# Performance work log

Hardware: AMD Instinct MI355X
Metric: run time of the kernel (lower is better)

The kernel has to match this reference:

```python
import jax, jax.numpy as jnp
import numpy as np

N_NODES = 100000
N_EDGES = 1_600_000
IN_DIM, HID, OUT_DIM, N_BLOCKS = 963, 192, 3, 6


def spmm(src, dst, w, x):
    # sparse adj @ x, adj[dst, src] = w  (COO edge list)
    msgs = x[src] * w[:, None]                      # [E, F]
    return jax.ops.segment_sum(msgs, dst, num_segments=N_NODES)


def gconv(x, src, dst, ew, w, lw, b):
    # Pixel2Mesh GConv: adj @ (x @ W) + x @ W_loop + b
    return spmm(src, dst, ew, x @ w) + x @ lw + b


def setup_inputs() -> dict:
    key = jax.random.key(0)
    ks = jax.random.split(key, 13)
    s = 0.02  # small init scale to keep deep stack numerically tame
    return {
        "inputs": jax.random.normal(ks[0], (N_NODES, IN_DIM), jnp.float32),
        "edge_src": jax.random.randint(ks[1], (N_EDGES,), 0, N_NODES),
        "edge_dst": jax.random.randint(ks[2], (N_EDGES,), 0, N_NODES),
        "edge_weight": jax.random.uniform(ks[3], (N_EDGES,), jnp.float32) / 16.0,
        "w_in": jax.random.normal(ks[4], (IN_DIM, HID), jnp.float32) * s,
        "loop_in": jax.random.normal(ks[5], (IN_DIM, HID), jnp.float32) * s,
        "b_in": jnp.zeros((HID,), jnp.float32),
        "blocks_w": jax.random.normal(ks[6], (N_BLOCKS, 2, HID, HID), jnp.float32) * s,
        "blocks_loop": jax.random.normal(ks[7], (N_BLOCKS, 2, HID, HID), jnp.float32) * s,
        "blocks_b": jnp.zeros((N_BLOCKS, 2, HID), jnp.float32),
        "w_out": jax.random.normal(ks[8], (HID, OUT_DIM), jnp.float32) * s,
        "loop_out": jax.random.normal(ks[9], (HID, OUT_DIM), jnp.float32) * s,
        "b_out": jnp.zeros((OUT_DIM,), jnp.float32),
    }


def reference(inputs, edge_src, edge_dst, edge_weight, w_in, loop_in, b_in,
              blocks_w, blocks_loop, blocks_b, w_out, loop_out, b_out):
    x = gconv(inputs, edge_src, edge_dst, edge_weight, w_in, loop_in, b_in)

    def block(x, params):
        bw, bl, bb = params
        h = gconv(x, edge_src, edge_dst, edge_weight, bw[0], bl[0], bb[0])
        h = gconv(h, edge_src, edge_dst, edge_weight, bw[1], bl[1], bb[1])
        return (x + h) * 0.5, None

    x_cat, _ = jax.lax.scan(block, x, (blocks_w, blocks_loop, blocks_b))
    x_out = gconv(x_cat, edge_src, edge_dst, edge_weight, w_out, loop_out, b_out)
    return (x_out, x_cat)
```

## Files before the change

### kernel.cpp

```cpp
#include <hip/hip_runtime.h>
#include <cstdint>
#include <cstddef>

#define N_NODES 100000
#define N_EDGES 1600000
#define IN_DIM 963
#define HID 192
#define OUT_DIM 3

typedef _Float16 f16x8 __attribute__((ext_vector_type(8)));
typedef float f32x4 __attribute__((ext_vector_type(4)));

__global__ void count_kernel(const int* __restrict__ dst, int* __restrict__ counts, int E) {
    int i = blockIdx.x * blockDim.x + threadIdx.x;
    if (i < E) atomicAdd(&counts[dst[i]], 1);
}

__global__ void scan_kernel(const int* __restrict__ counts, int* __restrict__ row_ptr, int n) {
    __shared__ int buf[1024];
    __shared__ int carry_s;
    int t = threadIdx.x;
    if (t == 0) { carry_s = 0; row_ptr[0] = 0; }
    __syncthreads();
    for (int base = 0; base < n; base += 1024) {
        int idx = base + t;
        int v = (idx < n) ? counts[idx] : 0;
        buf[t] = v;
        __syncthreads();
        for (int off = 1; off < 1024; off <<= 1) {
            int add = (t >= off) ? buf[t - off] : 0;
            __syncthreads();
            buf[t] += add;
            __syncthreads();
        }
        int carry = carry_s;
        if (idx < n) row_ptr[idx + 1] = carry + buf[t];
        __syncthreads();
        if (t == 1023) carry_s = carry + buf[1023];
        __syncthreads();
    }
}

__global__ void copy_cursor_kernel(const int* __restrict__ rp, int* __restrict__ cursor, int n) {
    int i = blockIdx.x * blockDim.x + threadIdx.x;
    if (i < n) cursor[i] = rp[i];
}

__global__ void scatter_kernel(const int* __restrict__ src, const int* __restrict__ dst,
                               const float* __restrict__ w, int* __restrict__ cursor,
                               int* __restrict__ csr_src, float* __restrict__ csr_w,
                               int* __restrict__ csr_eid, int E) {
    int i = blockIdx.x * blockDim.x + threadIdx.x;
    if (i < E) {
        int d = dst[i];
        int p = atomicAdd(&cursor[d], 1);
        csr_src[p] = src[i];
        csr_w[p] = w[i];
        csr_eid[p] = i;
    }
}

__global__ void sortrow_kernel(const int* __restrict__ rp, int* __restrict__ csr_src,
                               float* __restrict__ csr_w, int* __restrict__ csr_eid, int n) {
    int r = blockIdx.x * blockDim.x + threadIdx.x;
    if (r >= n) return;
    int s = rp[r], e = rp[r + 1];
    for (int i = s + 1; i < e; ++i) {
        int ke = csr_eid[i]; int ks = csr_src[i]; float kw = csr_w[i];
        int j = i - 1;
        while (j >= s && csr_eid[j] > ke) {
            csr_eid[j + 1] = csr_eid[j];
            csr_src[j + 1] = csr_src[j];
            csr_w[j + 1] = csr_w[j];
            --j;
        }
        csr_eid[j + 1] = ke; csr_src[j + 1] = ks; csr_w[j + 1] = kw;
    }
}

__global__ __launch_bounds__(256)
void trans_split(const float* __restrict__ W, const float* __restrict__ L,
                 int K, int Kp, _Float16* __restrict__ out_hi, _Float16* __restrict__ out_lo) {
    __shared__ float tile[32][33];
    const int n0 = blockIdx.x * 32, k0 = blockIdx.y * 32;
    const int tx = threadIdx.x, ty = threadIdx.y;
#pragma unroll
    for (int i = 0; i < 4; ++i) {
        int k = k0 + ty + i * 8;
        int n = n0 + tx;
        float v = 0.f;
        if (k < K) v = (n < HID) ? W[(size_t)k * HID + n] : L[(size_t)k * HID + (n - HID)];
        tile[ty + i * 8][tx] = v;
    }
    __syncthreads();
#pragma unroll
    for (int i = 0; i < 4; ++i) {
        int nl = ty + i * 8;
        int n = n0 + nl;
        int k = k0 + tx;
        float v = tile[tx][nl];
        _Float16 hi = (_Float16)v;
        _Float16 lo = (_Float16)(v - (float)hi);
        out_hi[(size_t)n * Kp + k] = hi;
        out_lo[(size_t)n * Kp + k] = lo;
    }
}

__global__ __launch_bounds__(512, 1)
void gemm_mfma(const float* __restrict__ X, int M, int Kx, int Kp,
               const _Float16* __restrict__ Wth, const _Float16* __restrict__ Wtl,
               const float* __restrict__ bias, const float* __restrict__ res,
               float* __restrict__ Hdst, float* __restrict__ Tdst) {
    __shared__ __align__(16) _Float16 Ah[4096];
    __shared__ __align__(16) _Float16 Al[4096];
    __shared__ __align__(16) _Float16 Bh[12288];
    __shared__ __align__(16) _Float16 Bl[12288];

    const int m0 = blockIdx.x * 128;
    const int tid = threadIdx.x;
    const int lane = tid & 63;
    const int wave = tid >> 6;
    const int wr = wave >> 2;
    const int wc = wave & 3;

    const int q  = tid >> 2;
    const int kg = tid & 3;
    const int xr = (kg ^ q ^ (q >> 2)) & 3;
    const int arow = m0 + q;
    const bool arok = arow < M;
    const float* xrow = X + (size_t)(arok ? arow : 0) * Kx;

    float pa[8];
    f16x8 pbh[3], pbl[3];

    auto loadA = [&](int k0) {
        int kb = k0 + kg * 8;
        if (arok && kb + 8 <= Kx) {
            f32x4 v0 = *(const f32x4*)(xrow + kb);
            f32x4 v1 = *(const f32x4*)(xrow + kb + 4);
#pragma unroll
            for (int j = 0; j < 4; ++j) { pa[j] = v0[j]; pa[4 + j] = v1[j]; }
        } else {
#pragma unroll
            for (int j = 0; j < 8; ++j)
                pa[j] = (arok && kb + j < Kx) ? xrow[kb + j] : 0.f;
        }
    };
    auto loadB = [&](int k0) {
#pragma unroll
        for (int c = 0; c < 3; ++c) {
            size_t o = (size_t)(c * 128 + q) * Kp + k0 + kg * 8;
            pbh[c] = *(const f16x8*)(Wth + o);
            pbl[c] = *(const f16x8*)(Wtl + o);
        }
    };
    auto stash = [&]() {
        f16x8 hi, lo;
#pragma unroll
        for (int j = 0; j < 8; ++j) {
            float x = pa[j];
            _Float16 h = (_Float16)x;
            hi[j] = h;
            lo[j] = (_Float16)(x - (float)h);
        }
        const int aoff = q * 64 + xr * 16;
        *(f16x8*)((char*)Ah + aoff) = hi;
        *(f16x8*)((char*)Al + aoff) = lo;
#pragma unroll
        for (int c = 0; c < 3; ++c) {
            const int boff = (c * 128 + q) * 64 + xr * 16;
            *(f16x8*)((char*)Bh + boff) = pbh[c];
            *(f16x8*)((char*)Bl + boff) = pbl[c];
        }
    };

    int a_off[4], b_off[6];
#pragma unroll
    for (int mi = 0; mi < 4; ++mi) {
        int idx = wr * 64 + mi * 16 + (lane & 15);
        a_off[mi] = idx * 64 + ((((lane >> 4)) ^ idx ^ (idx >> 2)) & 3) * 16;
    }
#pragma unroll
    for (int ni = 0; ni < 6; ++ni) {
        int idx = wc * 96 + ni * 16 + (lane & 15);
        b_off[ni] = idx * 64 + ((((lane >> 4)) ^ idx ^ (idx >> 2)) & 3) * 16;
    }

    f32x4 acc[4][6];
#pragma unroll
    for (int i = 0; i < 4; ++i)
#pragma unroll
        for (int j = 0; j < 6; ++j)
            acc[i][j] = f32x4{0.f, 0.f, 0.f, 0.f};

    const int nsteps = (Kx + 31) / 32;
    loadA(0); loadB(0);
    stash();
    __syncthreads();

    for (int s = 0; s < nsteps; ++s) {
        const int k0 = s * 32;
        const bool more = (s + 1) < nsteps;
        if (more) { loadA(k0 + 32); loadB(k0 + 32); }

        f16x8 ah[4], al[4];
#pragma unroll
        for (int mi = 0; mi < 4; ++mi) {
            ah[mi] = *(const f16x8*)((char*)Ah + a_off[mi]);
            al[mi] = *(const f16x8*)((char*)Al + a_off[mi]);
        }
#pragma unroll
        for (int ni = 0; ni < 6; ++ni) {
            f16x8 bh = *(const f16x8*)((char*)Bh + b_off[ni]);
            f16x8 bl = *(const f16x8*)((char*)Bl + b_off[ni]);
#pragma unroll
            for (int mi = 0; mi < 4; ++mi)
                acc[mi][ni] = __builtin_amdgcn_mfma_f32_16x16x32_f16(ah[mi], bh, acc[mi][ni], 0, 0, 0);
#pragma unroll
            for (int mi = 0; mi < 4; ++mi)
                acc[mi][ni] = __builtin_amdgcn_mfma_f32_16x16x32_f16(al[mi], bh, acc[mi][ni], 0, 0, 0);
#pragma unroll
            for (int mi = 0; mi < 4; ++mi)
                acc[mi][ni] = __builtin_amdgcn_mfma_f32_16x16x32_f16(ah[mi], bl, acc[mi][ni], 0, 0, 0);
        }
        if (more) {
            __syncthreads();
            stash();
            __syncthreads();
        }
    }

    const bool isH = (wc < 2);
#pragma unroll
    for (int mi = 0; mi < 4; ++mi) {
        const int rbase = m0 + wr * 64 + mi * 16 + ((lane >> 4) << 2);
#pragma unroll
        for (int ni = 0; ni < 6; ++ni) {
            const int gc = wc * 96 + ni * 16 + (lane & 15);
            f32x4 v = acc[mi][ni];
            if (isH) {
#pragma unroll
                for (int j = 0; j < 4; ++j) {
                    int row = rbase + j;
                    if (row < M) Hdst[(size_t)row * HID + gc] = v[j];
                }
            } else {
                const int c = gc - HID;
                const float bv = bias[c];
#pragma unroll
                for (int j = 0; j < 4; ++j) {
                    int row = rbase + j;
                    if (row < M) {
                        float t = v[j] + bv;
                        if (res != nullptr) t += res[(size_t)row * HID + c];
                        Tdst[(size_t)row * HID + c] = t;
                    }
                }
            }
        }
    }
}

__global__ __launch_bounds__(256)
void spmm_kernel(const int* __restrict__ rp, const int* __restrict__ csrc,
                 const float* __restrict__ cw, const float* __restrict__ Hm,
                 float* __restrict__ out, float scale) {
    int wid = (blockIdx.x * 256 + threadIdx.x) >> 6;
    int lane = threadIdx.x & 63;
    if (wid >= N_NODES) return;
    int s = rp[wid], e = rp[wid + 1];
    float a0 = 0.f, a1 = 0.f, a2 = 0.f;
    int i = s;
    for (; i + 3 < e; i += 4) {
        float w0 = cw[i], w1 = cw[i + 1], w2 = cw[i + 2], w3 = cw[i + 3];
        const float* h0 = Hm + (size_t)csrc[i] * HID;
        const float* h1 = Hm + (size_t)csrc[i + 1] * HID;
        const float* h2 = Hm + (size_t)csrc[i + 2] * HID;
        const float* h3 = Hm + (size_t)csrc[i + 3] * HID;
        float x00 = h0[lane], x01 = h0[64 + lane], x02 = h0[128 + lane];
        float x10 = h1[lane], x11 = h1[64 + lane], x12 = h1[128 + lane];
        float x20 = h2[lane], x21 = h2[64 + lane], x22 = h2[128 + lane];
        float x30 = h3[lane], x31 = h3[64 + lane], x32 = h3[128 + lane];
        a0 += w0 * x00; a1 += w0 * x01; a2 += w0 * x02;
        a0 += w1 * x10; a1 += w1 * x11; a2 += w1 * x12;
        a0 += w2 * x20; a1 += w2 * x21; a2 += w2 * x22;
        a0 += w3 * x30; a1 += w3 * x31; a2 += w3 * x32;
    }
    for (; i < e; ++i) {
        float w = cw[i];
        const float* h = Hm + (size_t)csrc[i] * HID;
        a0 += w * h[lane];
        a1 += w * h[64 + lane];
        a2 += w * h[128 + lane];
    }
    float* o = out + (size_t)wid * HID;
    o[lane]       = scale * (o[lane] + a0);
    o[64 + lane]  = scale * (o[64 + lane] + a1);
    o[128 + lane] = scale * (o[128 + lane] + a2);
}

__global__ __launch_bounds__(256)
void out_gemm(const float* __restrict__ X, const float* __restrict__ Wout,
              const float* __restrict__ Lout, const float* __restrict__ bout,
              float* __restrict__ H3, float* __restrict__ T3) {
    __shared__ float Ws[HID * OUT_DIM];
    __shared__ float Ls[HID * OUT_DIM];
    int tid = threadIdx.x;
    for (int i = tid; i < HID * OUT_DIM; i += 256) { Ws[i] = Wout[i]; Ls[i] = Lout[i]; }
    __syncthreads();
    int n = blockIdx.x * 4 + (tid >> 6);
    int lane = tid & 63;
    if (n >= N_NODES) return;
    const float* x = X + (size_t)n * HID;
    float aw[3] = {0.f, 0.f, 0.f}, al[3] = {0.f, 0.f, 0.f};
#pragma unroll
    for (int p = 0; p < 3; ++p) {
        int k = p * 64 + lane;
        float xv = x[k];
#pragma unroll
        for (int c = 0; c < 3; ++c) {
            aw[c] += xv * Ws[k * 3 + c];
            al[c] += xv * Ls[k * 3 + c];
        }
    }
#pragma unroll
    for (int off = 32; off > 0; off >>= 1) {
#pragma unroll
        for (int c = 0; c < 3; ++c) {
            aw[c] += __shfl_down(aw[c], off, 64);
            al[c] += __shfl_down(al[c], off, 64);
        }
    }
    if (lane == 0) {
#pragma unroll
        for (int c = 0; c < 3; ++c) {
            H3[n * 3 + c] = aw[c];
            T3[n * 3 + c] = al[c] + bout[c];
        }
    }
}

__global__ __launch_bounds__(256)
void out_spmm(const int* __restrict__ rp, const int* __restrict__ csrc,
              const float* __restrict__ cw, const float* __restrict__ H3,
              const float* __restrict__ T3, float* __restrict__ out) {
    int n = blockIdx.x * blockDim.x + threadIdx.x;
    if (n >= N_NODES) return;
    int s = rp[n], e = rp[n + 1];
    float a0 = 0.f, a1 = 0.f, a2 = 0.f;
    for (int i = s; i < e; ++i) {
        float w = cw[i];
        int src = csrc[i];
        a0 += w * H3[src * 3 + 0];
        a1 += w * H3[src * 3 + 1];
        a2 += w * H3[src * 3 + 2];
    }
    out[n * 3 + 0] = a0 + T3[n * 3 + 0];
    out[n * 3 + 1] = a1 + T3[n * 3 + 1];
    out[n * 3 + 2] = a2 + T3[n * 3 + 2];
}

extern "C" void kernel_launch(void* const* d_in, const int* in_sizes, int n_in,
                              void* d_out, int out_size, void* d_ws, size_t ws_size,
                              hipStream_t stream) {
    const float* X0    = (const float*)d_in[0];
    const int*   esrc  = (const int*)d_in[1];
    const int*   edst  = (const int*)d_in[2];
    const float* ew    = (const float*)d_in[3];
    const float* w_in  = (const float*)d_in[4];
    const float* l_in  = (const float*)d_in[5];
    const float* b_in  = (const float*)d_in[6];
    const float* bw    = (const float*)d_in[7];
    const float* bl    = (const float*)d_in[8];
    const float* bb    = (const float*)d_in[9];
    const float* w_out = (const float*)d_in[10];
    const float* l_out = (const float*)d_in[11];
    const float* b_out = (const float*)d_in[12];

    char* ws = (char*)d_ws;
    size_t off = 0;
    auto alloc = [&](size_t bytes) -> void* {
        void* p = ws + off;
        off += (bytes + 255) & ~(size_t)255;
        return p;
    };
    float* Hbuf   = (float*)alloc(sizeof(float) * (size_t)N_NODES * HID);
    float* h1     = (float*)alloc(sizeof(float) * (size_t)N_NODES * HID);
    int*   counts = (int*)alloc(sizeof(int) * N_NODES);
    int*   rp     = (int*)alloc(sizeof(int) * (N_NODES + 1));
    int*   cursor = (int*)alloc(sizeof(int) * N_NODES);
    int*   csrc   = (int*)alloc(sizeof(int) * N_EDGES);
    float* cw     = (float*)alloc(sizeof(float) * N_EDGES);
    int*   ceid   = (int*)alloc(sizeof(int) * N_EDGES);
    float* H3     = (float*)alloc(sizeof(float) * (size_t)N_NODES * OUT_DIM);
    float* T3     = (float*)alloc(sizeof(float) * (size_t)N_NODES * OUT_DIM);
    const int KP0 = 992;
    _Float16* Wt0h = (_Float16*)alloc(sizeof(_Float16) * 384 * KP0);
    _Float16* Wt0l = (_Float16*)alloc(sizeof(_Float16) * 384 * KP0);
    _Float16* WtHh = (_Float16*)alloc(sizeof(_Float16) * 12 * 384 * HID);
    _Float16* WtHl = (_Float16*)alloc(sizeof(_Float16) * 12 * 384 * HID);

    float* xout = (float*)d_out;
    float* xcat = (float*)d_out + (size_t)N_NODES * OUT_DIM;

    trans_split<<<dim3(12, 31), dim3(32, 8), 0, stream>>>(w_in, l_in, IN_DIM, KP0, Wt0h, Wt0l);
    for (int l = 0; l < 12; ++l) {
        trans_split<<<dim3(12, 6), dim3(32, 8), 0, stream>>>(
            bw + (size_t)l * HID * HID, bl + (size_t)l * HID * HID, HID, HID,
            WtHh + (size_t)l * 384 * HID, WtHl + (size_t)l * 384 * HID);
    }

    hipMemsetAsync(counts, 0, sizeof(int) * N_NODES, stream);
    count_kernel<<<(N_EDGES + 255) / 256, 256, 0, stream>>>(edst, counts, N_EDGES);
    scan_kernel<<<1, 1024, 0, stream>>>(counts, rp, N_NODES);
    copy_cursor_kernel<<<(N_NODES + 255) / 256, 256, 0, stream>>>(rp, cursor, N_NODES);
    scatter_kernel<<<(N_EDGES + 255) / 256, 256, 0, stream>>>(esrc, edst, ew, cursor,
                                                              csrc, cw, ceid, N_EDGES);
    sortrow_kernel<<<(N_NODES + 255) / 256, 256, 0, stream>>>(rp, csrc, cw, ceid, N_NODES);

    const int gemm_blocks = (N_NODES + 127) / 128;
    const int spmm_blocks = (N_NODES * 64 + 255) / 256;

    gemm_mfma<<<gemm_blocks, 512, 0, stream>>>(X0, N_NODES, IN_DIM, KP0, Wt0h, Wt0l,
                                               b_in, nullptr, Hbuf, xcat);
    spmm_kernel<<<spmm_blocks, 256, 0, stream>>>(rp, csrc, cw, Hbuf, xcat, 1.0f);

    for (int b = 0; b < 6; ++b) {
        int l0 = b * 2, l1 = b * 2 + 1;
        const float* B0 = bb + (size_t)l0 * HID;
        const float* B1 = bb + (size_t)l1 * HID;

        gemm_mfma<<<gemm_blocks, 512, 0, stream>>>(xcat, N_NODES, HID, HID,
                                                   WtHh + (size_t)l0 * 384 * HID,
                                                   WtHl + (size_t)l0 * 384 * HID,
                                                   B0, nullptr, Hbuf, h1);
        spmm_kernel<<<spmm_blocks, 256, 0, stream>>>(rp, csrc, cw, Hbuf, h1, 1.0f);
        gemm_mfma<<<gemm_blocks, 512, 0, stream>>>(h1, N_NODES, HID, HID,
                                                   WtHh + (size_t)l1 * 384 * HID,
                                                   WtHl + (size_t)l1 * 384 * HID,
                                                   B1, xcat, Hbuf, xcat);
        spmm_kernel<<<spmm_blocks, 256, 0, stream>>>(rp, csrc, cw, Hbuf, xcat, 0.5f);
    }

    out_gemm<<<(N_NODES + 3) / 4, 256, 0, stream>>>(xcat, w_out, l_out, b_out, H3, T3);
    out_spmm<<<(N_NODES + 255) / 256, 256, 0, stream>>>(rp, csrc, cw, H3, T3, xout);
}
```

Measured before the change: 5.217 ms.

## Split GEMM columns across grid, double-buffer LDS, and unroll SpMM by eight

The fused MFMA GEMM now splits its 384 output columns across two grid columns, using 256-thread blocks with two blocks per CU instead of one 512-thread block. Its LDS tiles are double-buffered, so there is one barrier per K-step instead of two, letting global loads for the next step overlap the MFMA work. The SpMM gather loop is unrolled by eight to keep more independent row loads in flight. The cost is that each X row is now read by two blocks, which doubles A-operand traffic and is heaviest for the 963-wide input layer.

Result: faster. 4.651 ms (-10.8%).

```diff
diff --git a/kernel.cpp b/kernel.cpp
--- a/kernel.cpp
+++ b/kernel.cpp
@@ -106,84 +106,95 @@
     }
 }
 
-__global__ __launch_bounds__(512, 1)
+__global__ __launch_bounds__(256, 2)
 void gemm_mfma(const float* __restrict__ X, int M, int Kx, int Kp,
                const _Float16* __restrict__ Wth, const _Float16* __restrict__ Wtl,
                const float* __restrict__ bias, const float* __restrict__ res,
                float* __restrict__ Hdst, float* __restrict__ Tdst) {
-    __shared__ __align__(16) _Float16 Ah[4096];
-    __shared__ __align__(16) _Float16 Al[4096];
-    __shared__ __align__(16) _Float16 Bh[12288];
-    __shared__ __align__(16) _Float16 Bl[12288];
+    __shared__ __align__(16) _Float16 Ah[2][4096];
+    __shared__ __align__(16) _Float16 Al[2][4096];
+    __shared__ __align__(16) _Float16 Bh[2][6144];
+    __shared__ __align__(16) _Float16 Bl[2][6144];
 
     const int m0 = blockIdx.x * 128;
+    const int bcol = blockIdx.y * 192;
     const int tid = threadIdx.x;
     const int lane = tid & 63;
     const int wave = tid >> 6;
-    const int wr = wave >> 2;
-    const int wc = wave & 3;
-
-    const int q  = tid >> 2;
-    const int kg = tid & 3;
-    const int xr = (kg ^ q ^ (q >> 2)) & 3;
-    const int arow = m0 + q;
+    const int wr = wave >> 1;
+    const int wc = wave & 1;
+
+    const int ar = tid >> 1;
+    const int ah_ = tid & 1;
+    const int arow = m0 + ar;
     const bool arok = arow < M;
     const float* xrow = X + (size_t)(arok ? arow : 0) * Kx;
 
-    float pa[8];
+    float pa[16];
     f16x8 pbh[3], pbl[3];
 
     auto loadA = [&](int k0) {
-        int kb = k0 + kg * 8;
-        if (arok && kb + 8 <= Kx) {
-            f32x4 v0 = *(const f32x4*)(xrow + kb);
-            f32x4 v1 = *(const f32x4*)(xrow + kb + 4);
-#pragma unroll
-            for (int j = 0; j < 4; ++j) { pa[j] = v0[j]; pa[4 + j] = v1[j]; }
+        const int kb = k0 + ah_ * 16;
+        if (arok && kb + 16 <= Kx) {
+#pragma unroll
+            for (int c = 0; c < 4; ++c) {
+                f32x4 v = *(const f32x4*)(xrow + kb + c * 4);
+#pragma unroll
+                for (int j = 0; j < 4; ++j) pa[c * 4 + j] = v[j];
+            }
         } else {
 #pragma unroll
-            for (int j = 0; j < 8; ++j)
+            for (int j = 0; j < 16; ++j)
                 pa[j] = (arok && kb + j < Kx) ? xrow[kb + j] : 0.f;
         }
     };
     auto loadB = [&](int k0) {
 #pragma unroll
         for (int c = 0; c < 3; ++c) {
-            size_t o = (size_t)(c * 128 + q) * Kp + k0 + kg * 8;
+            const int id = c * 256 + tid;
+            const int idx = id >> 2, kg = id & 3;
+            const size_t o = (size_t)(bcol + idx) * Kp + k0 + kg * 8;
             pbh[c] = *(const f16x8*)(Wth + o);
             pbl[c] = *(const f16x8*)(Wtl + o);
         }
     };
-    auto stash = [&]() {
-        f16x8 hi, lo;
-#pragma unroll
-        for (int j = 0; j < 8; ++j) {
-            float x = pa[j];
-            _Float16 h = (_Float16)x;
-            hi[j] = h;
-            lo[j] = (_Float16)(x - (float)h);
-        }
-        const int aoff = q * 64 + xr * 16;
-        *(f16x8*)((char*)Ah + aoff) = hi;
-        *(f16x8*)((char*)Al + aoff) = lo;
+    auto stash = [&](int b) {
+#pragma unroll
+        for (int c = 0; c < 2; ++c) {
+            const int kg = ah_ * 2 + c;
+            f16x8 hi, lo;
+#pragma unroll
+            for (int j = 0; j < 8; ++j) {
+                float x = pa[c * 8 + j];
+                _Float16 h = (_Float16)x;
+                hi[j] = h;
+                lo[j] = (_Float16)(x - (float)h);
+            }
+            const int off = ar * 64 + ((kg ^ ar ^ (ar >> 2)) & 3) * 16;
+            *(f16x8*)((char*)&Ah[b][0] + off) = hi;
+            *(f16x8*)((char*)&Al[b][0] + off) = lo;
+        }
 #pragma unroll
         for (int c = 0; c < 3; ++c) {
-            const int boff = (c * 128 + q) * 64 + xr * 16;
-            *(f16x8*)((char*)Bh + boff) = pbh[c];
-            *(f16x8*)((char*)Bl + boff) = pbl[c];
+            const int id = c * 256 + tid;
+            const int idx = id >> 2, kg = id & 3;
+            const int off = idx * 64 + ((kg ^ idx ^ (idx >> 2)) & 3) * 16;
+            *(f16x8*)((char*)&Bh[b][0] + off) = pbh[c];
+            *(f16x8*)((char*)&Bl[b][0] + off) = pbl[c];
         }
     };
 
     int a_off[4], b_off[6];
+    const int kgl = lane >> 4;
 #pragma unroll
     for (int mi = 0; mi < 4; ++mi) {
-        int idx = wr * 64 + mi * 16 + (lane & 15);
-        a_off[mi] = idx * 64 + ((((lane >> 4)) ^ idx ^ (idx >> 2)) & 3) * 16;
+        const int idx = wr * 64 + mi * 16 + (lane & 15);
+        a_off[mi] = idx * 64 + ((kgl ^ idx ^ (idx >> 2)) & 3) * 16;
     }
 #pragma unroll
     for (int ni = 0; ni < 6; ++ni) {
-        int idx = wc * 96 + ni * 16 + (lane & 15);
-        b_off[ni] = idx * 64 + ((((lane >> 4)) ^ idx ^ (idx >> 2)) & 3) * 16;
+        const int idx = wc * 96 + ni * 16 + (lane & 15);
+        b_off[ni] = idx * 64 + ((kgl ^ idx ^ (idx >> 2)) & 3) * 16;
     }
 
     f32x4 acc[4][6];
@@ -195,42 +206,38 @@
 
     const int nsteps = (Kx + 31) / 32;
     loadA(0); loadB(0);
-    stash();
-    __syncthreads();
 
     for (int s = 0; s < nsteps; ++s) {
-        const int k0 = s * 32;
-        const bool more = (s + 1) < nsteps;
-        if (more) { loadA(k0 + 32); loadB(k0 + 32); }
-
-        f16x8 ah[4], al[4];
+        const int b = s & 1;
+        stash(b);
+        if (s + 1 < nsteps) { loadA((s + 1) * 32); loadB((s + 1) * 32); }
+        asm volatile("s_waitcnt lgkmcnt(0)" ::: "memory");
+        __builtin_amdgcn_s_barrier();
+        __builtin_amdgcn_sched_barrier(0);
+
+        f16x8 fah[4], fal[4];
 #pragma unroll
         for (int mi = 0; mi < 4; ++mi) {
-            ah[mi] = *(const f16x8*)((char*)Ah + a_off[mi]);
-            al[mi] = *(const f16x8*)((char*)Al + a_off[mi]);
+            fah[mi] = *(const f16x8*)((char*)&Ah[b][0] + a_off[mi]);
+            fal[mi] = *(const f16x8*)((char*)&Al[b][0] + a_off[mi]);
         }
 #pragma unroll
         for (int ni = 0; ni < 6; ++ni) {
-            f16x8 bh = *(const f16x8*)((char*)Bh + b_off[ni]);
-            f16x8 bl = *(const f16x8*)((char*)Bl + b_off[ni]);
+            const f16x8 fbh = *(const f16x8*)((char*)&Bh[b][0] + b_off[ni]);
+            const f16x8 fbl = *(const f16x8*)((char*)&Bl[b][0] + b_off[ni]);
 #pragma unroll
             for (int mi = 0; mi < 4; ++mi)
-                acc[mi][ni] = __builtin_amdgcn_mfma_f32_16x16x32_f16(ah[mi], bh, acc[mi][ni], 0, 0, 0);
+                acc[mi][ni] = __builtin_amdgcn_mfma_f32_16x16x32_f16(fah[mi], fbh, acc[mi][ni], 0, 0, 0);
 #pragma unroll
             for (int mi = 0; mi < 4; ++mi)
-                acc[mi][ni] = __builtin_amdgcn_mfma_f32_16x16x32_f16(al[mi], bh, acc[mi][ni], 0, 0, 0);
+                acc[mi][ni] = __builtin_amdgcn_mfma_f32_16x16x32_f16(fal[mi], fbh, acc[mi][ni], 0, 0, 0);
 #pragma unroll
             for (int mi = 0; mi < 4; ++mi)
-                acc[mi][ni] = __builtin_amdgcn_mfma_f32_16x16x32_f16(ah[mi], bl, acc[mi][ni], 0, 0, 0);
-        }
-        if (more) {
-            __syncthreads();
-            stash();
-            __syncthreads();
-        }
-    }
-
-    const bool isH = (wc < 2);
+                acc[mi][ni] = __builtin_amdgcn_mfma_f32_16x16x32_f16(fah[mi], fbl, acc[mi][ni], 0, 0, 0);
+        }
+    }
+
+    const bool isH = (bcol == 0);
 #pragma unroll
     for (int mi = 0; mi < 4; ++mi) {
         const int rbase = m0 + wr * 64 + mi * 16 + ((lane >> 4) << 2);
@@ -241,19 +248,18 @@
             if (isH) {
 #pragma unroll
                 for (int j = 0; j < 4; ++j) {
-                    int row = rbase + j;
+                    const int row = rbase + j;
                     if (row < M) Hdst[(size_t)row * HID + gc] = v[j];
                 }
             } else {
-                const int c = gc - HID;
-                const float bv = bias[c];
+                const float bv = bias[gc];
 #pragma unroll
                 for (int j = 0; j < 4; ++j) {
-                    int row = rbase + j;
+                    const int row = rbase + j;
                     if (row < M) {
                         float t = v[j] + bv;
-                        if (res != nullptr) t += res[(size_t)row * HID + c];
-                        Tdst[(size_t)row * HID + c] = t;
+                        if (res != nullptr) t += res[(size_t)row * HID + gc];
+                        Tdst[(size_t)row * HID + gc] = t;
                     }
                 }
             }
@@ -271,20 +277,33 @@
     int s = rp[wid], e = rp[wid + 1];
     float a0 = 0.f, a1 = 0.f, a2 = 0.f;
     int i = s;
+    for (; i + 7 < e; i += 8) {
+        float w[8];
+        const float* h[8];
+#pragma unroll
+        for (int u = 0; u < 8; ++u) {
+            w[u] = cw[i + u];
+            h[u] = Hm + (size_t)csrc[i + u] * HID;
+        }
+#pragma unroll
+        for (int u = 0; u < 8; ++u) {
+            float x0 = h[u][lane], x1 = h[u][64 + lane], x2 = h[u][128 + lane];
+            a0 += w[u] * x0; a1 += w[u] * x1; a2 += w[u] * x2;
+        }
+    }
     for (; i + 3 < e; i += 4) {
-        float w0 = cw[i], w1 = cw[i + 1], w2 = cw[i + 2], w3 = cw[i + 3];
-        const float* h0 = Hm + (size_t)csrc[i] * HID;
-        const float* h1 = Hm + (size_t)csrc[i + 1] * HID;
-        const float* h2 = Hm + (size_t)csrc[i + 2] * HID;
-        const float* h3 = Hm + (size_t)csrc[i + 3] * HID;
-        float x00 = h0[lane], x01 = h0[64 + lane], x02 = h0[128 + lane];
-        float x10 = h1[lane], x11 = h1[64 + lane], x12 = h1[128 + lane];
-        float x20 = h2[lane], x21 = h2[64 + lane], x22 = h2[128 + lane];
-        float x30 = h3[lane], x31 = h3[64 + lane], x32 = h3[128 + lane];
-        a0 += w0 * x00; a1 += w0 * x01; a2 += w0 * x02;
-        a0 += w1 * x10; a1 += w1 * x11; a2 += w1 * x12;
-        a0 += w2 * x20; a1 += w2 * x21; a2 += w2 * x22;
-        a0 += w3 * x30; a1 += w3 * x31; a2 += w3 * x32;
+        float w[4];
+        const float* h[4];
+#pragma unroll
+        for (int u = 0; u < 4; ++u) {
+            w[u] = cw[i + u];
+            h[u] = Hm + (size_t)csrc[i + u] * HID;
+        }
+#pragma unroll
+        for (int u = 0; u < 4; ++u) {
+            float x0 = h[u][lane], x1 = h[u][64 + lane], x2 = h[u][128 + lane];
+            a0 += w[u] * x0; a1 += w[u] * x1; a2 += w[u] * x2;
+        }
     }
     for (; i < e; ++i) {
         float w = cw[i];
@@ -418,11 +437,11 @@
                                                               csrc, cw, ceid, N_EDGES);
     sortrow_kernel<<<(N_NODES + 255) / 256, 256, 0, stream>>>(rp, csrc, cw, ceid, N_NODES);
 
-    const int gemm_blocks = (N_NODES + 127) / 128;
+    const dim3 gemm_grid((N_NODES + 127) / 128, 2);
     const int spmm_blocks = (N_NODES * 64 + 255) / 256;
 
-    gemm_mfma<<<gemm_blocks, 512, 0, stream>>>(X0, N_NODES, IN_DIM, KP0, Wt0h, Wt0l,
-                                               b_in, nullptr, Hbuf, xcat);
+    gemm_mfma<<<gemm_grid, 256, 0, stream>>>(X0, N_NODES, IN_DIM, KP0, Wt0h, Wt0l,
+                                             b_in, nullptr, Hbuf, xcat);
     spmm_kernel<<<spmm_blocks, 256, 0, stream>>>(rp, csrc, cw, Hbuf, xcat, 1.0f);
 
     for (int b = 0; b < 6; ++b) {
@@ -430,15 +449,15 @@
         const float* B0 = bb + (size_t)l0 * HID;
         const float* B1 = bb + (size_t)l1 * HID;
 
-        gemm_mfma<<<gemm_blocks, 512, 0, stream>>>(xcat, N_NODES, HID, HID,
-                                                   WtHh + (size_t)l0 * 384 * HID,
-                                                   WtHl + (size_t)l0 * 384 * HID,
-                                                   B0, nullptr, Hbuf, h1);
+        gemm_mfma<<<gemm_grid, 256, 0, stream>>>(xcat, N_NODES, HID, HID,
+                                                 WtHh + (size_t)l0 * 384 * HID,
+                                                 WtHl + (size_t)l0 * 384 * HID,
+                                                 B0, nullptr, Hbuf, h1);
         spmm_kernel<<<spmm_blocks, 256, 0, stream>>>(rp, csrc, cw, Hbuf, h1, 1.0f);
-        gemm_mfma<<<gemm_blocks, 512, 0, stream>>>(h1, N_NODES, HID, HID,
-                                                   WtHh + (size_t)l1 * 384 * HID,
-                                                   WtHl + (size_t)l1 * 384 * HID,
-                                                   B1, xcat, Hbuf, xcat);
+        gemm_mfma<<<gemm_grid, 256, 0, stream>>>(h1, N_NODES, HID, HID,
+                                                 WtHh + (size_t)l1 * 384 * HID,
+                                                 WtHl + (size_t)l1 * 384 * HID,
+                                                 B1, xcat, Hbuf, xcat);
         spmm_kernel<<<spmm_blocks, 256, 0, stream>>>(rp, csrc, cw, Hbuf, xcat, 0.5f);
     }
 
```
